# Kernel optimization log

Measured on AMD Instinct MI355X. Metric: run time of the kernel, lower is better.

The kernel has to match this reference:

```python
import jax, jax.numpy as jnp
import numpy as np
from math import sqrt

B, LQ, LKV = 4, 1024, 1024
QD = KD = VD = 1024
MODEL_DIM = 1024
H = 16
HD = MODEL_DIM // H  # per-head model_dim = 64


def setup_inputs() -> dict:
    key = jax.random.key(0)
    ks = jax.random.split(key, 10)
    s = 0.02
    return {
        "queries": jax.random.normal(ks[0], (B, LQ, QD), jnp.float32),
        "context": jax.random.normal(ks[1], (B, LKV, KD), jnp.float32),
        # stacked per-head linear weights (torch Linear: y = x @ W.T + b); store as [H, in, out]
        "Wq": jax.random.normal(ks[2], (H, QD, HD), jnp.float32) * s,
        "bq": jax.random.normal(ks[3], (H, HD), jnp.float32) * s,
        "Wk": jax.random.normal(ks[4], (KD, HD * 1 * H), jnp.float32).reshape(H, KD, HD) * s,
        "bk": jax.random.normal(ks[5], (H, HD), jnp.float32) * s,
        "Wv": jax.random.normal(ks[6], (H, VD, HD), jnp.float32) * s,
        "bv": jax.random.normal(ks[7], (H, HD), jnp.float32) * s,
        "Wo": jax.random.normal(ks[8], (H * HD, MODEL_DIM), jnp.float32) * s,
        "bo": jax.random.normal(ks[9], (MODEL_DIM,), jnp.float32) * s,
    }


def reference(queries, context, Wq, bq, Wk, bk, Wv, bv, Wo, bo):
    # queries: [B,Lq,Dq]; context: [B,Lkv,Dk]
    # Per-head projections, batched over heads (equivalent to the torch per-head loop).
    q = jnp.einsum("bld,hdm->bhlm", queries, Wq) + bq[None, :, None, :]  # [B,H,Lq,hd]
    k = jnp.einsum("bld,hdm->bhlm", context, Wk) + bk[None, :, None, :]  # [B,H,Lkv,hd]
    v = jnp.einsum("bld,hdm->bhlm", context, Wv) + bv[None, :, None, :]  # [B,H,Lkv,hd]

    scale = 1.0 / sqrt(HD)
    scores = jnp.einsum("bhqd,bhkd->bhqk", q, k) * scale  # [B,H,Lq,Lkv]
    att = jax.nn.softmax(scores, axis=-1)
    head_out = jnp.einsum("bhqk,bhkd->bhqd", att, v)  # [B,H,Lq,hd]

    # torch concatenates heads along the last dim in head order 0..H-1
    multi = head_out.transpose(0, 2, 1, 3).reshape(B, LQ, H * HD)
    residual = q.transpose(0, 2, 1, 3).reshape(B, LQ, H * HD)

    out = multi @ Wo + bo  # [B,Lq,model_dim]
    return out, residual
```

## Files before the change

kernel.cpp:

```cpp
#include <hip/hip_runtime.h>
#include <hip/hip_bf16.h>


typedef unsigned short u16;
typedef __attribute__((ext_vector_type(8))) short short8;
typedef __attribute__((ext_vector_type(4))) float f32x4;

__device__ __forceinline__ float bf2f(u16 u) {
    union { unsigned int i; float f; } c;
    c.i = ((unsigned int)u) << 16;
    return c.f;
}

__device__ __forceinline__ u16 f2bf(float f) {
    unsigned int x = __float_as_uint(f);
    unsigned int r = (x + 0x7fffu + ((x >> 16) & 1u)) >> 16;
    return (u16)r;
}

__device__ __forceinline__ void glds16(u16* lds, const u16* g) {
    __builtin_amdgcn_global_load_lds(
        (const __attribute__((address_space(1))) void*)g,
        (__attribute__((address_space(3))) void*)lds, 16, 0, 0);
}

__global__ __launch_bounds__(256) void prep(
    const float* __restrict__ q, const float* __restrict__ ctx,
    const float* __restrict__ Wq, const float* __restrict__ Wk,
    const float* __restrict__ Wv, const float* __restrict__ Wo,
    u16* __restrict__ Aq, u16* __restrict__ Ac,
    u16* __restrict__ Wqt, u16* __restrict__ Wkt,
    u16* __restrict__ Wvt, u16* __restrict__ Wot)
{
    __shared__ float ls[64][65];
    const int t = threadIdx.x;
    int bid = blockIdx.x;

    if (bid < 4096) {
        const float* in = (bid < 2048) ? q : ctx;
        u16* out = (bid < 2048) ? Aq : Ac;
        size_t i = ((size_t)(bid & 2047) * 256 + t) * 8;
        float4 v0 = *(const float4*)(in + i);
        float4 v1 = *(const float4*)(in + i + 4);
        short8 p;
        p[0] = (short)f2bf(v0.x); p[1] = (short)f2bf(v0.y);
        p[2] = (short)f2bf(v0.z); p[3] = (short)f2bf(v0.w);
        p[4] = (short)f2bf(v1.x); p[5] = (short)f2bf(v1.y);
        p[6] = (short)f2bf(v1.z); p[7] = (short)f2bf(v1.w);
        *(short8*)(out + i) = p;
        return;
    }
    bid -= 4096;
    const float* in; u16* out; int C; size_t moff; int rt, ct;
    if (bid < 768) {
        const int m = bid >> 8, idx = bid & 255;
        in = (m == 0) ? Wq : (m == 1) ? Wk : Wv;
        out = (m == 0) ? Wqt : (m == 1) ? Wkt : Wvt;
        C = 64; rt = (idx & 15) * 64; ct = 0; moff = (size_t)(idx >> 4) * 65536;
    } else {
        const int idx = bid - 768;
        in = Wo; out = Wot; C = 1024; moff = 0;
        rt = (idx & 15) * 64; ct = (idx >> 4) * 64;
    }
    #pragma unroll
    for (int i = 0; i < 4; ++i) {
        int s = i * 256 + t;
        int row = s >> 4, chunk = s & 15;
        float4 v = *(const float4*)(in + moff + (size_t)(rt + row) * C + ct + chunk * 4);
        ls[row][chunk * 4 + 0] = v.x;
        ls[row][chunk * 4 + 1] = v.y;
        ls[row][chunk * 4 + 2] = v.z;
        ls[row][chunk * 4 + 3] = v.w;
    }
    __syncthreads();
    #pragma unroll
    for (int i = 0; i < 2; ++i) {
        int s = i * 256 + t;
        int n = s >> 3, kc = s & 7;
        short8 p;
        #pragma unroll
        for (int j = 0; j < 8; ++j) p[j] = (short)f2bf(ls[kc * 8 + j][n]);
        *(short8*)(out + moff + (size_t)(ct + n) * 1024 + rt + kc * 8) = p;
    }
}

__global__ __launch_bounds__(256) void gemm_qkv(
    const u16* __restrict__ Aq, const u16* __restrict__ Ac,
    const u16* __restrict__ Wqt, const u16* __restrict__ Wkt,
    const u16* __restrict__ Wvt,
    const float* __restrict__ bq, const float* __restrict__ bk,
    const float* __restrict__ bv,
    u16* __restrict__ qws, u16* __restrict__ kws, u16* __restrict__ vtws)
{
    __shared__ u16 As[128 * 64];
    __shared__ u16 Bs[128 * 64];
    const int n0 = blockIdx.x * 128, m0 = blockIdx.y * 128, z = blockIdx.z;
    const int t = threadIdx.x;
    const int w = t >> 6, lane = t & 63;
    const int quad = lane >> 4, c = lane & 15;
    const int cx = c & 7;

    const u16* A = (z == 0) ? Aq : Ac;
    const u16* Wt = ((z == 0) ? Wqt : (z == 1) ? Wkt : Wvt) + (size_t)n0 * 1024;
    const float* bias = (z == 0) ? bq : (z == 1) ? bk : bv;

    const int sr = w * 8 + (lane >> 3);
    const int gch = (lane & 7) ^ ((lane >> 3) & 7);
    const u16* gA = A + (size_t)(m0 + sr) * 1024 + gch * 8;
    const u16* gB = Wt + (size_t)sr * 1024 + gch * 8;

    const int arow = (w >> 1) * 64 + c;
    const int brow = (w & 1) * 64 + c;

    f32x4 acc[4][4] = {};

    for (int kt = 0; kt < 1024; kt += 64) {
        #pragma unroll
        for (int i = 0; i < 4; ++i) {
            glds16(As + (i * 32 + w * 8) * 64, gA + (size_t)i * 32 * 1024 + kt);
            glds16(Bs + (i * 32 + w * 8) * 64, gB + (size_t)i * 32 * 1024 + kt);
        }
        __syncthreads();
        #pragma unroll
        for (int kh = 0; kh < 2; ++kh) {
            const int ch = (kh * 4 + quad);
            short8 af[4], bf[4];
            #pragma unroll
            for (int rs = 0; rs < 4; ++rs)
                af[rs] = *(const short8*)(As + (arow + rs * 16) * 64 + (ch ^ cx) * 8);
            #pragma unroll
            for (int cs = 0; cs < 4; ++cs)
                bf[cs] = *(const short8*)(Bs + (brow + cs * 16) * 64 + (ch ^ cx) * 8);
            #pragma unroll
            for (int rs = 0; rs < 4; ++rs)
                #pragma unroll
                for (int cs = 0; cs < 4; ++cs)
                    acc[rs][cs] = __builtin_amdgcn_mfma_f32_16x16x32_bf16(
                        af[rs], bf[cs], acc[rs][cs], 0, 0, 0);
        }
        __syncthreads();
    }

    const int h = blockIdx.x * 2 + (w & 1);
    float bb[4];
    #pragma unroll
    for (int cs = 0; cs < 4; ++cs) bb[cs] = bias[h * 64 + cs * 16 + c];

    if (z == 2) {
        #pragma unroll
        for (int rs = 0; rs < 4; ++rs) {
            const int l0 = m0 + (w >> 1) * 64 + rs * 16 + quad * 4;
            const int b = l0 >> 10, l = l0 & 1023;
            #pragma unroll
            for (int cs = 0; cs < 4; ++cs) {
                const int hd = cs * 16 + c;
                ushort4 pk;
                pk.x = f2bf(acc[rs][cs][0] + bb[cs]);
                pk.y = f2bf(acc[rs][cs][1] + bb[cs]);
                pk.z = f2bf(acc[rs][cs][2] + bb[cs]);
                pk.w = f2bf(acc[rs][cs][3] + bb[cs]);
                *(ushort4*)(vtws + ((size_t)(b * 16 + h) * 64 + hd) * 1024 + l) = pk;
            }
        }
    } else {
        u16* dst = (z == 0) ? qws : kws;
        const float scale = (z == 0) ? 0.125f : 1.0f;
        #pragma unroll
        for (int rs = 0; rs < 4; ++rs)
            #pragma unroll
            for (int r = 0; r < 4; ++r) {
                const int row = m0 + (w >> 1) * 64 + rs * 16 + quad * 4 + r;
                const int b = row >> 10, l = row & 1023;
                u16* drow = dst + (((size_t)(b * 16 + h) * 1024) + l) * 64;
                #pragma unroll
                for (int cs = 0; cs < 4; ++cs)
                    drow[cs * 16 + c] = f2bf((acc[rs][cs][r] + bb[cs]) * scale);
            }
    }
}

__global__ __launch_bounds__(256) void gemm_out(
    const u16* __restrict__ A, const u16* __restrict__ Wot,
    const float* __restrict__ bo, float* __restrict__ out)
{
    __shared__ u16 As[128 * 64];
    __shared__ u16 Bs[64 * 64];
    const int f = blockIdx.x;
    const int xcd = f & 7, k = f >> 3;
    const int m0 = (xcd * 4 + (k & 3)) * 128;
    const int n0 = (k >> 2) * 64;
    const int t = threadIdx.x;
    const int w = t >> 6, lane = t & 63;
    const int quad = lane >> 4, c = lane & 15;
    const int cx = c & 7;

    const int sr = w * 8 + (lane >> 3);
    const int gch = (lane & 7) ^ ((lane >> 3) & 7);
    const u16* gA = A + (size_t)(m0 + sr) * 1024 + gch * 8;
    const u16* gB = Wot + (size_t)(n0 + sr) * 1024 + gch * 8;

    const int arow = (w >> 1) * 64 + c;
    const int brow = (w & 1) * 32 + c;

    f32x4 acc[4][2] = {};
    for (int kt = 0; kt < 1024; kt += 64) {
        #pragma unroll
        for (int i = 0; i < 4; ++i)
            glds16(As + (i * 32 + w * 8) * 64, gA + (size_t)i * 32 * 1024 + kt);
        #pragma unroll
        for (int i = 0; i < 2; ++i)
            glds16(Bs + (i * 32 + w * 8) * 64, gB + (size_t)i * 32 * 1024 + kt);
        __syncthreads();
        #pragma unroll
        for (int kh = 0; kh < 2; ++kh) {
            const int ch = (kh * 4 + quad);
            short8 af[4], bf[2];
            #pragma unroll
            for (int rs = 0; rs < 4; ++rs)
                af[rs] = *(const short8*)(As + (arow + rs * 16) * 64 + (ch ^ cx) * 8);
            #pragma unroll
            for (int cs = 0; cs < 2; ++cs)
                bf[cs] = *(const short8*)(Bs + (brow + cs * 16) * 64 + (ch ^ cx) * 8);
            #pragma unroll
            for (int rs = 0; rs < 4; ++rs)
                #pragma unroll
                for (int cs = 0; cs < 2; ++cs)
                    acc[rs][cs] = __builtin_amdgcn_mfma_f32_16x16x32_bf16(
                        af[rs], bf[cs], acc[rs][cs], 0, 0, 0);
        }
        __syncthreads();
    }

    const int nb = n0 + (w & 1) * 32;
    float bb[2];
    #pragma unroll
    for (int cs = 0; cs < 2; ++cs) bb[cs] = bo[nb + cs * 16 + c];

    #pragma unroll
    for (int rs = 0; rs < 4; ++rs) {
        #pragma unroll
        for (int r = 0; r < 4; ++r) {
            const int row = m0 + (w >> 1) * 64 + rs * 16 + quad * 4 + r;
            float* orow = out + (size_t)row * 1024 + nb;
            #pragma unroll
            for (int cs = 0; cs < 2; ++cs)
                orow[cs * 16 + c] = acc[rs][cs][r] + bb[cs];
        }
    }
}

__global__ __launch_bounds__(256) void attn_mfma(
    const u16* __restrict__ qws, const u16* __restrict__ kws,
    const u16* __restrict__ vtws, u16* __restrict__ multi,
    float* __restrict__ resid)
{
    __shared__ u16 Ks[64 * 64];
    __shared__ u16 Vs[64 * 64];
    __shared__ u16 Ps[4][16 * 72];
    const int t = threadIdx.x;
    const int wave = t >> 6, lane = t & 63;
    const int quad = lane >> 4, c = lane & 15;
    const int f = blockIdx.x;
    const int xcd = f & 7, j = f >> 3;
    const int bh = xcd * 8 + (j & 7);
    const int qt = j >> 3;
    const int b = bh >> 4, h = bh & 15;
    const int q0 = qt * 64 + wave * 16;

    const u16* qb = qws + ((size_t)bh * 1024 + q0) * 64;
    const u16* kb = kws + (size_t)bh * 65536;
    const u16* vb = vtws + (size_t)bh * 65536;

    short8 qa0 = *(const short8*)(qb + (size_t)c * 64 + quad * 8);
    short8 qa1 = *(const short8*)(qb + (size_t)c * 64 + 32 + quad * 8);

    const int srow = wave * 16 + (lane >> 3);
    const int gch = (lane & 7) ^ ((lane >> 3) & 7);
    u16* ldsK0 = Ks + (wave * 16) * 64;
    u16* ldsK1 = Ks + (wave * 16 + 8) * 64;
    u16* ldsV0 = Vs + (wave * 16) * 64;
    u16* ldsV1 = Vs + (wave * 16 + 8) * 64;
    const u16* gK0 = kb + (size_t)srow * 64 + gch * 8;
    const u16* gK1 = kb + (size_t)(srow + 8) * 64 + gch * 8;
    const u16* gV0 = vb + (size_t)srow * 1024 + gch * 8;
    const u16* gV1 = vb + (size_t)(srow + 8) * 1024 + gch * 8;

    f32x4 O[4] = {};
    float ps[4] = {0.f, 0.f, 0.f, 0.f};
    u16* pw = &Ps[wave][0];
    const int cx = c & 7;

    for (int kt = 0; kt < 1024; kt += 64) {
        glds16(ldsK0, gK0 + (size_t)kt * 64);
        glds16(ldsK1, gK1 + (size_t)kt * 64);
        glds16(ldsV0, gV0 + kt);
        glds16(ldsV1, gV1 + kt);
        __syncthreads();

        f32x4 s[4];
        #pragma unroll
        for (int nt = 0; nt < 4; ++nt) {
            const u16* kr = Ks + (nt * 16 + c) * 64;
            short8 kb0 = *(const short8*)(kr + ((quad ^ cx)) * 8);
            short8 kb1 = *(const short8*)(kr + (((4 + quad) ^ cx)) * 8);
            f32x4 z = {};
            z = __builtin_amdgcn_mfma_f32_16x16x32_bf16(qa0, kb0, z, 0, 0, 0);
            z = __builtin_amdgcn_mfma_f32_16x16x32_bf16(qa1, kb1, z, 0, 0, 0);
            s[nt] = z;
        }

        #pragma unroll
        for (int nt = 0; nt < 4; ++nt)
            #pragma unroll
            for (int r = 0; r < 4; ++r) {
                float p = __expf(s[nt][r]);
                ps[r] += p;
                pw[(quad * 4 + r) * 72 + nt * 16 + c] = (u16)(__float_as_uint(p) >> 16);
            }
        short8 pa0 = *(const short8*)(pw + c * 72 + quad * 8);
        short8 pa1 = *(const short8*)(pw + c * 72 + 32 + quad * 8);

        #pragma unroll
        for (int nt = 0; nt < 4; ++nt) {
            const u16* vr = Vs + (nt * 16 + c) * 64;
            short8 vb0 = *(const short8*)(vr + ((quad ^ cx)) * 8);
            short8 vb1 = *(const short8*)(vr + (((4 + quad) ^ cx)) * 8);
            O[nt] = __builtin_amdgcn_mfma_f32_16x16x32_bf16(pa0, vb0, O[nt], 0, 0, 0);
            O[nt] = __builtin_amdgcn_mfma_f32_16x16x32_bf16(pa1, vb1, O[nt], 0, 0, 0);
        }
        __syncthreads();
    }

    float inv[4];
    #pragma unroll
    for (int r = 0; r < 4; ++r) {
        float sum = ps[r];
        sum += __shfl_xor(sum, 1);
        sum += __shfl_xor(sum, 2);
        sum += __shfl_xor(sum, 4);
        sum += __shfl_xor(sum, 8);
        inv[r] = 1.0f / sum;
    }

    u16* ob = multi + ((size_t)b * 1024 + q0 + quad * 4) * 1024 + h * 64 + c;
    #pragma unroll
    for (int r = 0; r < 4; ++r) {
        u16* orow = ob + (size_t)r * 1024;
        orow[0]  = f2bf(O[0][r] * inv[r]);
        orow[16] = f2bf(O[1][r] * inv[r]);
        orow[32] = f2bf(O[2][r] * inv[r]);
        orow[48] = f2bf(O[3][r] * inv[r]);
    }

    float* rr = resid + ((size_t)b * 1024 + q0 + c) * 1024 + h * 64;
    #pragma unroll
    for (int jj = 0; jj < 8; ++jj) {
        rr[quad * 8 + jj]      = bf2f((u16)qa0[jj]) * 8.0f;
        rr[32 + quad * 8 + jj] = bf2f((u16)qa1[jj]) * 8.0f;
    }
}

extern "C" void kernel_launch(void* const* d_in, const int* in_sizes, int n_in,
                              void* d_out, int out_size, void* d_ws, size_t ws_size,
                              hipStream_t stream) {
    const float* queries = (const float*)d_in[0];
    const float* context = (const float*)d_in[1];
    const float* Wq = (const float*)d_in[2];
    const float* bq = (const float*)d_in[3];
    const float* Wk = (const float*)d_in[4];
    const float* bk = (const float*)d_in[5];
    const float* Wv = (const float*)d_in[6];
    const float* bv = (const float*)d_in[7];
    const float* Wo = (const float*)d_in[8];
    const float* bo = (const float*)d_in[9];

    float* out = (float*)d_out;
    float* resid = out + (size_t)4 * 1024 * 1024;

    const size_t M1 = 1024 * 1024;
    u16* Aq   = (u16*)d_ws;
    u16* Ac   = Aq + 4 * M1;
    u16* Wqt  = Ac + 4 * M1;
    u16* Wkt  = Wqt + M1;
    u16* Wvt  = Wkt + M1;
    u16* Wot  = Wvt + M1;
    u16* qws  = Wot + M1;
    u16* kws  = qws + 4 * M1;
    u16* vtws = kws + 4 * M1;
    u16* mws  = vtws + 4 * M1;

    prep<<<5120, 256, 0, stream>>>(queries, context, Wq, Wk, Wv, Wo,
                                   Aq, Ac, Wqt, Wkt, Wvt, Wot);
    gemm_qkv<<<dim3(8, 32, 3), 256, 0, stream>>>(Aq, Ac, Wqt, Wkt, Wvt,
                                                 bq, bk, bv, qws, kws, vtws);
    attn_mfma<<<1024, 256, 0, stream>>>(qws, kws, vtws, mws, resid);
    gemm_out<<<512, 256, 0, stream>>>(mws, Wot, bo, out);
}
```

Baseline: 202.0 us.

## Rewrite QKV projection GEMM as 256x256 tile, 8-wave, double-buffered pipelined kernel

Replaces the 128x128 single-buffered QKV GEMM with a 512-thread kernel computing 256x256 tiles. The K loop is double-buffered in LDS, with global-to-LDS loads for the next stage interleaved between quarter-tile MFMA blocks under explicit barriers, vmcnt/lgkmcnt waits and setprio. Blocks are remapped so that neighbouring M tiles land on the same XCD. The aim is to hide load latency and raise data reuse per block. The cost is 128KB of LDS and 128 accumulator registers per thread, leaving only 192 blocks and low occupancy.

```diff
diff --git a/kernel.cpp b/kernel.cpp
--- a/kernel.cpp
+++ b/kernel.cpp
@@ -23,6 +23,15 @@
         (const __attribute__((address_space(1))) void*)g,
         (__attribute__((address_space(3))) void*)lds, 16, 0, 0);
 }
+
+#define FENCE() asm volatile("" ::: "memory")
+#define BAR() do { FENCE(); __builtin_amdgcn_s_barrier(); FENCE(); } while (0)
+#define WAIT_LGKM0() do { asm volatile("s_waitcnt lgkmcnt(0)" ::: "memory"); \
+                          __builtin_amdgcn_sched_barrier(0); } while (0)
+#define WAIT_VM4() do { asm volatile("s_waitcnt vmcnt(4)" ::: "memory"); \
+                        __builtin_amdgcn_sched_barrier(0); } while (0)
+#define WAIT_VM0() do { asm volatile("s_waitcnt vmcnt(0)" ::: "memory"); \
+                        __builtin_amdgcn_sched_barrier(0); } while (0)
 
 __global__ __launch_bounds__(256) void prep(
     const float* __restrict__ q, const float* __restrict__ ctx,
@@ -84,7 +93,7 @@
     }
 }
 
-__global__ __launch_bounds__(256) void gemm_qkv(
+__global__ __launch_bounds__(512) void gemm_qkv8(
     const u16* __restrict__ Aq, const u16* __restrict__ Ac,
     const u16* __restrict__ Wqt, const u16* __restrict__ Wkt,
     const u16* __restrict__ Wvt,
@@ -92,90 +101,167 @@
     const float* __restrict__ bv,
     u16* __restrict__ qws, u16* __restrict__ kws, u16* __restrict__ vtws)
 {
-    __shared__ u16 As[128 * 64];
-    __shared__ u16 Bs[128 * 64];
-    const int n0 = blockIdx.x * 128, m0 = blockIdx.y * 128, z = blockIdx.z;
-    const int t = threadIdx.x;
-    const int w = t >> 6, lane = t & 63;
-    const int quad = lane >> 4, c = lane & 15;
-    const int cx = c & 7;
+    __shared__ u16 lds[2][2][256 * 64];
+
+    const int tid = threadIdx.x;
+    const int w = tid >> 6, lane = tid & 63;
+    const int wr = w >> 2, wc = w & 3;
+    const int quad = lane >> 4, c = lane & 15, cx = c & 7;
+    const int sr = tid >> 3;
+    const int gch = (tid & 7) ^ (sr & 7);
+
+    const int f = blockIdx.x;
+    const int xcd = f & 7, r = f >> 3;
+    const int z = r >> 3;
+    const int mt = xcd * 2 + ((r >> 2) & 1);
+    const int nt = r & 3;
+    const int m0 = mt * 256, n0 = nt * 256;
 
     const u16* A = (z == 0) ? Aq : Ac;
-    const u16* Wt = ((z == 0) ? Wqt : (z == 1) ? Wkt : Wvt) + (size_t)n0 * 1024;
+    const u16* Wt = (z == 0) ? Wqt : (z == 1) ? Wkt : Wvt;
     const float* bias = (z == 0) ? bq : (z == 1) ? bk : bv;
 
-    const int sr = w * 8 + (lane >> 3);
-    const int gch = (lane & 7) ^ ((lane >> 3) & 7);
-    const u16* gA = A + (size_t)(m0 + sr) * 1024 + gch * 8;
-    const u16* gB = Wt + (size_t)sr * 1024 + gch * 8;
-
-    const int arow = (w >> 1) * 64 + c;
-    const int brow = (w & 1) * 64 + c;
-
-    f32x4 acc[4][4] = {};
-
-    for (int kt = 0; kt < 1024; kt += 64) {
-        #pragma unroll
-        for (int i = 0; i < 4; ++i) {
-            glds16(As + (i * 32 + w * 8) * 64, gA + (size_t)i * 32 * 1024 + kt);
-            glds16(Bs + (i * 32 + w * 8) * 64, gB + (size_t)i * 32 * 1024 + kt);
-        }
-        __syncthreads();
-        #pragma unroll
-        for (int kh = 0; kh < 2; ++kh) {
-            const int ch = (kh * 4 + quad);
-            short8 af[4], bf[4];
-            #pragma unroll
-            for (int rs = 0; rs < 4; ++rs)
-                af[rs] = *(const short8*)(As + (arow + rs * 16) * 64 + (ch ^ cx) * 8);
-            #pragma unroll
-            for (int cs = 0; cs < 4; ++cs)
-                bf[cs] = *(const short8*)(Bs + (brow + cs * 16) * 64 + (ch ^ cx) * 8);
-            #pragma unroll
-            for (int rs = 0; rs < 4; ++rs)
+    const u16* gAt = A + (size_t)(m0 + sr) * 1024 + gch * 8;
+    const u16* gBt = Wt + (size_t)(n0 + sr) * 1024 + gch * 8;
+
+    auto stageA = [&](int par, int half, int t) {
+        const u16* g = gAt + (size_t)half * 128 * 1024 + t * 64;
+        u16* l = &lds[par][0][(half * 128 + w * 8) * 64];
+        glds16(l, g);
+        glds16(l + 64 * 64, g + (size_t)64 * 1024);
+    };
+    auto stageB = [&](int par, int half, int t) {
+        const u16* g = gBt + (size_t)half * 128 * 1024 + t * 64;
+        u16* l = &lds[par][1][(half * 128 + w * 8) * 64];
+        glds16(l, g);
+        glds16(l + 64 * 64, g + (size_t)64 * 1024);
+    };
+
+    f32x4 acc[8][4] = {};
+    short8 aq[4][2], bA[2][2], bB[2][2];
+
+    auto ldA = [&](int par, int mh) {
+        #pragma unroll
+        for (int mf = 0; mf < 4; ++mf)
+            #pragma unroll
+            for (int ks = 0; ks < 2; ++ks)
+                aq[mf][ks] = *(const short8*)&lds[par][0][
+                    (wr * 128 + mh * 64 + mf * 16 + c) * 64 + (((ks * 4 + quad) ^ cx) * 8)];
+    };
+    auto ldB = [&](int par, int nh, short8 (&bq_)[2][2]) {
+        #pragma unroll
+        for (int nf = 0; nf < 2; ++nf)
+            #pragma unroll
+            for (int ks = 0; ks < 2; ++ks)
+                bq_[nf][ks] = *(const short8*)&lds[par][1][
+                    (wc * 64 + nh * 32 + nf * 16 + c) * 64 + (((ks * 4 + quad) ^ cx) * 8)];
+    };
+    auto mma = [&](int mh, int nh, short8 (&bq_)[2][2]) {
+        #pragma unroll
+        for (int mf = 0; mf < 4; ++mf)
+            #pragma unroll
+            for (int nf = 0; nf < 2; ++nf)
                 #pragma unroll
-                for (int cs = 0; cs < 4; ++cs)
-                    acc[rs][cs] = __builtin_amdgcn_mfma_f32_16x16x32_bf16(
-                        af[rs], bf[cs], acc[rs][cs], 0, 0, 0);
-        }
-        __syncthreads();
-    }
-
-    const int h = blockIdx.x * 2 + (w & 1);
+                for (int ks = 0; ks < 2; ++ks)
+                    acc[mh * 4 + mf][nh * 2 + nf] =
+                        __builtin_amdgcn_mfma_f32_16x16x32_bf16(
+                            aq[mf][ks], bq_[nf][ks], acc[mh * 4 + mf][nh * 2 + nf], 0, 0, 0);
+    };
+
+    stageB(0, 0, 0); stageB(0, 1, 0); stageA(0, 0, 0); stageA(0, 1, 0);
+    stageB(1, 0, 1); stageB(1, 1, 1);
+    WAIT_VM4(); BAR();
+
+    #pragma unroll 1
+    for (int i = 0; i < 8; ++i) {
+        const int o = 2 * i + 1, e = 2 * i + 2;
+
+        ldA(0, 0); ldB(0, 0, bA);
+        stageA(1, 0, o);
+        BAR(); WAIT_LGKM0();
+        __builtin_amdgcn_s_setprio(1); mma(0, 0, bA); __builtin_amdgcn_s_setprio(0);
+        BAR();
+        ldB(0, 1, bB);
+        stageA(1, 1, o);
+        BAR(); WAIT_LGKM0();
+        __builtin_amdgcn_s_setprio(1); mma(0, 1, bB); __builtin_amdgcn_s_setprio(0);
+        BAR();
+        ldA(0, 1);
+        if (i < 7) stageB(0, 0, e);
+        BAR(); WAIT_LGKM0();
+        __builtin_amdgcn_s_setprio(1); mma(1, 1, bB); __builtin_amdgcn_s_setprio(0);
+        BAR();
+        if (i < 7) stageB(0, 1, e);
+        BAR();
+        __builtin_amdgcn_s_setprio(1); mma(1, 0, bA); __builtin_amdgcn_s_setprio(0);
+        if (i < 7) { WAIT_VM4(); } else { WAIT_VM0(); }
+        BAR();
+        ldA(1, 0); ldB(1, 0, bA);
+        if (i < 7) stageA(0, 0, e);
+        BAR(); WAIT_LGKM0();
+        __builtin_amdgcn_s_setprio(1); mma(0, 0, bA); __builtin_amdgcn_s_setprio(0);
+        BAR();
+        ldB(1, 1, bB);
+        if (i < 7) stageA(0, 1, e);
+        BAR(); WAIT_LGKM0();
+        __builtin_amdgcn_s_setprio(1); mma(0, 1, bB); __builtin_amdgcn_s_setprio(0);
+        BAR();
+        ldA(1, 1);
+        if (i < 7) stageB(1, 0, e + 1);
+        BAR(); WAIT_LGKM0();
+        __builtin_amdgcn_s_setprio(1); mma(1, 1, bB); __builtin_amdgcn_s_setprio(0);
+        BAR();
+        if (i < 7) stageB(1, 1, e + 1);
+        BAR();
+        __builtin_amdgcn_s_setprio(1); mma(1, 0, bA); __builtin_amdgcn_s_setprio(0);
+        if (i < 7) WAIT_VM4();
+        BAR();
+    }
+
+    const int h = nt * 4 + wc;
+    const int b = m0 >> 10;
+    const int lbase = (m0 & 1023) + wr * 128;
+
     float bb[4];
     #pragma unroll
-    for (int cs = 0; cs < 4; ++cs) bb[cs] = bias[h * 64 + cs * 16 + c];
-
-    if (z == 2) {
-        #pragma unroll
-        for (int rs = 0; rs < 4; ++rs) {
-            const int l0 = m0 + (w >> 1) * 64 + rs * 16 + quad * 4;
-            const int b = l0 >> 10, l = l0 & 1023;
-            #pragma unroll
-            for (int cs = 0; cs < 4; ++cs) {
-                const int hd = cs * 16 + c;
-                ushort4 pk;
-                pk.x = f2bf(acc[rs][cs][0] + bb[cs]);
-                pk.y = f2bf(acc[rs][cs][1] + bb[cs]);
-                pk.z = f2bf(acc[rs][cs][2] + bb[cs]);
-                pk.w = f2bf(acc[rs][cs][3] + bb[cs]);
-                *(ushort4*)(vtws + ((size_t)(b * 16 + h) * 64 + hd) * 1024 + l) = pk;
-            }
-        }
-    } else {
+    for (int cn = 0; cn < 4; ++cn)
+        bb[cn] = bias[h * 64 + (cn >> 1) * 32 + (cn & 1) * 16 + c];
+
+    if (z < 2) {
         u16* dst = (z == 0) ? qws : kws;
         const float scale = (z == 0) ? 0.125f : 1.0f;
-        #pragma unroll
-        for (int rs = 0; rs < 4; ++rs)
-            #pragma unroll
-            for (int r = 0; r < 4; ++r) {
-                const int row = m0 + (w >> 1) * 64 + rs * 16 + quad * 4 + r;
-                const int b = row >> 10, l = row & 1023;
-                u16* drow = dst + (((size_t)(b * 16 + h) * 1024) + l) * 64;
+        u16* dbase = dst + (size_t)(b * 16 + h) * 1024 * 64;
+        #pragma unroll
+        for (int mi = 0; mi < 8; ++mi) {
+            const int ro = (mi >> 2) * 64 + (mi & 3) * 16;
+            const int rowb = lbase + ro + quad * 4;
+            #pragma unroll
+            for (int rr = 0; rr < 4; ++rr) {
+                u16* drow = dbase + (size_t)(rowb + rr) * 64;
                 #pragma unroll
-                for (int cs = 0; cs < 4; ++cs)
-                    drow[cs * 16 + c] = f2bf((acc[rs][cs][r] + bb[cs]) * scale);
+                for (int cn = 0; cn < 4; ++cn) {
+                    const int hd = (cn >> 1) * 32 + (cn & 1) * 16 + c;
+                    drow[hd] = f2bf((acc[mi][cn][rr] + bb[cn]) * scale);
+                }
             }
+        }
+    } else {
+        u16* dbase = vtws + (size_t)(b * 16 + h) * 64 * 1024;
+        #pragma unroll
+        for (int mi = 0; mi < 8; ++mi) {
+            const int ro = (mi >> 2) * 64 + (mi & 3) * 16;
+            const int l0 = lbase + ro + quad * 4;
+            #pragma unroll
+            for (int cn = 0; cn < 4; ++cn) {
+                const int hd = (cn >> 1) * 32 + (cn & 1) * 16 + c;
+                ushort4 pk;
+                pk.x = f2bf(acc[mi][cn][0] + bb[cn]);
+                pk.y = f2bf(acc[mi][cn][1] + bb[cn]);
+                pk.z = f2bf(acc[mi][cn][2] + bb[cn]);
+                pk.w = f2bf(acc[mi][cn][3] + bb[cn]);
+                *(ushort4*)(dbase + (size_t)hd * 1024 + l0) = pk;
+            }
+        }
     }
 }
 
@@ -391,8 +477,8 @@
 
     prep<<<5120, 256, 0, stream>>>(queries, context, Wq, Wk, Wv, Wo,
                                    Aq, Ac, Wqt, Wkt, Wvt, Wot);
-    gemm_qkv<<<dim3(8, 32, 3), 256, 0, stream>>>(Aq, Ac, Wqt, Wkt, Wvt,
-                                                 bq, bk, bv, qws, kws, vtws);
+    gemm_qkv8<<<192, 512, 0, stream>>>(Aq, Ac, Wqt, Wkt, Wvt,
+                                       bq, bk, bv, qws, kws, vtws);
     attn_mfma<<<1024, 256, 0, stream>>>(qws, kws, vtws, mws, resid);
     gemm_out<<<512, 256, 0, stream>>>(mws, Wot, bo, out);
 }
```

Result: faster. 194.2 us (-3.9%).
